# Optimization experiments

Measured on AMD Instinct MI355X. Metric: run time of the kernel, lower is better.

The kernel has to match this reference:

```python
import jax, jax.numpy as jnp
import numpy as np

B, S, DIN, DOUT = 4, 4096, 4096, 4096
W_SCALE = 0.02  # kaiming-ish scale; keeps values inside fp8 range


def setup_inputs() -> dict:
    key = jax.random.key(0)
    k1, k2, k3 = jax.random.split(key, 3)
    x = jax.random.normal(k1, (B, S, DIN), dtype=jnp.float16)
    weight = (jax.random.normal(k2, (DOUT, DIN), dtype=jnp.float32) * W_SCALE).astype(jnp.float16)
    bias = (jax.random.normal(k3, (DOUT,), dtype=jnp.float32) * W_SCALE).astype(jnp.float16)
    return {"x": x, "weight": weight, "bias": bias}


def reference(x, weight, bias):
    # Emulate torch._scaled_mm: activations quantized to fp8 e5m2,
    # weight (transposed) quantized to fp8 e4m3fn, scale_a = scale_b = 1.0,
    # accumulate in fp32, add fp16 bias, output fp16.
    out_shape = x.shape[:-1] + (weight.shape[0],)
    x8 = x.reshape(-1, x.shape[-1]).astype(jnp.float8_e5m2)       # [M, DIN]
    w8 = weight.T.astype(jnp.float8_e4m3fn)                        # [DIN, DOUT]
    scale = jnp.float32(1.0)  # scale_a * scale_b
    acc = jnp.matmul(x8.astype(jnp.float32), w8.astype(jnp.float32))  # [M, DOUT] fp32 accum
    out = (acc * scale + bias.astype(jnp.float32)).astype(jnp.float16)
    return out.reshape(out_shape)
```

## Files before the change

kernel.cpp:

```cpp
#include <hip/hip_runtime.h>
#include <hip/hip_fp16.h>

#define M_DIM 16384
#define N_DIM 4096
#define K_DIM 4096

typedef __attribute__((ext_vector_type(16))) float f32x16;
typedef __attribute__((ext_vector_type(4)))  int   i32x4;
typedef __attribute__((ext_vector_type(8)))  int   i32x8;

template<bool E4M3>
__global__ __launch_bounds__(256) void quant_tile_kernel(
    const float* __restrict__ in,
    uint4* __restrict__ out,
    int ngrp)
{
  int t = blockIdx.x * 256 + threadIdx.x;
  if (t >= ngrp) return;
  const int g    = t & 1023;
  const int tile = t >> 10;
  const int kt   = tile & 63;
  const int bt   = tile >> 6;
  const int sb   = g >> 7;
  const int half = (g >> 6) & 1;
  const int l    = g & 63;
  const int row  = bt * 256 + sb * 32 + (l & 31);
  const int k    = kt * 64 + (l >> 5) * 32 + half * 16;

  const float4* p = reinterpret_cast<const float4*>(in + (size_t)row * K_DIM + k);
  float4 v0 = p[0], v1 = p[1], v2 = p[2], v3 = p[3];
  int w0 = 0, w1 = 0, w2 = 0, w3 = 0;
  if (E4M3) {
    w0 = __builtin_amdgcn_cvt_pk_fp8_f32(v0.x, v0.y, w0, false);
    w0 = __builtin_amdgcn_cvt_pk_fp8_f32(v0.z, v0.w, w0, true);
    w1 = __builtin_amdgcn_cvt_pk_fp8_f32(v1.x, v1.y, w1, false);
    w1 = __builtin_amdgcn_cvt_pk_fp8_f32(v1.z, v1.w, w1, true);
    w2 = __builtin_amdgcn_cvt_pk_fp8_f32(v2.x, v2.y, w2, false);
    w2 = __builtin_amdgcn_cvt_pk_fp8_f32(v2.z, v2.w, w2, true);
    w3 = __builtin_amdgcn_cvt_pk_fp8_f32(v3.x, v3.y, w3, false);
    w3 = __builtin_amdgcn_cvt_pk_fp8_f32(v3.z, v3.w, w3, true);
  } else {
    w0 = __builtin_amdgcn_cvt_pk_bf8_f32(v0.x, v0.y, w0, false);
    w0 = __builtin_amdgcn_cvt_pk_bf8_f32(v0.z, v0.w, w0, true);
    w1 = __builtin_amdgcn_cvt_pk_bf8_f32(v1.x, v1.y, w1, false);
    w1 = __builtin_amdgcn_cvt_pk_bf8_f32(v1.z, v1.w, w1, true);
    w2 = __builtin_amdgcn_cvt_pk_bf8_f32(v2.x, v2.y, w2, false);
    w2 = __builtin_amdgcn_cvt_pk_bf8_f32(v2.z, v2.w, w2, true);
    w3 = __builtin_amdgcn_cvt_pk_bf8_f32(v3.x, v3.y, w3, false);
    w3 = __builtin_amdgcn_cvt_pk_bf8_f32(v3.z, v3.w, w3, true);
  }
  out[t] = make_uint4((unsigned)w0, (unsigned)w1, (unsigned)w2, (unsigned)w3);
}

__global__ __launch_bounds__(512, 2) void gemm_fp8_kernel(
    const unsigned char* __restrict__ Aq,
    const unsigned char* __restrict__ Wq,
    const float* __restrict__ bias,
    float* __restrict__ C)
{
  __shared__ __align__(16) unsigned char lds[98304];

  const int tid  = threadIdx.x;
  const int lane = tid & 63;
  const int wave = tid >> 6;
  const int wr   = wave >> 2;
  const int wc   = wave & 3;

  const int bid = blockIdx.x;
  const int swz = (bid & 7) * 128 + (bid >> 3);
  const int bmi = swz >> 4;
  const int bni = swz & 15;

  const unsigned char* tA = Aq + (size_t)bmi * (64 * 16384);
  const unsigned char* tB = Wq + (size_t)bni * (64 * 16384);

  const size_t t16 = (size_t)tid * 16;
  const int    w1k = wave * 1024;

#define STAGE(gb, lo_)                                                      \
  __builtin_amdgcn_global_load_lds(                                        \
      (const __attribute__((address_space(1))) void*)((gb) + t16),          \
      (__attribute__((address_space(3))) void*)(lds + (lo_) + w1k), 16, 0, 0)

#define RD8(dst, off)                                                       \
  { const unsigned char* _p = lds + (off) + lane * 16;                      \
    union { i32x8 v; i32x4 h[2]; } _u;                                      \
    _u.h[0] = *(const i32x4*)_p;                                            \
    _u.h[1] = *(const i32x4*)(_p + 1024);                                   \
    (dst) = _u.v; }

#define MFMA(d, a, b)                                                       \
  d = __builtin_amdgcn_mfma_scale_f32_32x32x64_f8f6f4(                      \
      a, b, d, 1 , 0 , 0, 0x7F7F7F7F, 0, 0x7F7F7F7F)

#define SBAR __builtin_amdgcn_sched_barrier(0)
#define BAR  __builtin_amdgcn_s_barrier()
#define DSW  asm volatile("s_waitcnt lgkmcnt(0)" ::: "memory"); SBAR
#define VMW4 asm volatile("s_waitcnt vmcnt(4)" ::: "memory"); SBAR
#define P1   __builtin_amdgcn_s_setprio(1)
#define P0   __builtin_amdgcn_s_setprio(0)

  const int aoff = wr * 8192;
  const int boff = 16384 + wc * 4096;

  f32x16 acc[4][2] = {};
  i32x8 aU, aV, bE0, bE1, bO0, bO1;

  STAGE(tA,         0);      STAGE(tA + 8192,  8192);
  STAGE(tB,         16384);  STAGE(tB + 8192,  24576);
  SBAR;
  STAGE(tA + 16384, 32768);  STAGE(tA + 24576, 40960);
  STAGE(tB + 16384, 49152);  STAGE(tB + 24576, 57344);
  SBAR;
  VMW4;
  BAR;

  int cA = 0, cB = 32768, cC = 65536;

  for (int it = 0; it < 32; ++it) {
    const int t = it << 1;
    const size_t tpC = (size_t)((t + 2) & 63) * 16384;
    const size_t tpD = (size_t)((t + 3) & 63) * 16384;

    RD8(bE0, cA + boff);  RD8(bE1, cA + boff + 2048);
    RD8(aU,  cA + aoff);
    STAGE(tA + tpC, cC);
    BAR; DSW; P1;
    MFMA(acc[0][0], aU, bE0); MFMA(acc[0][1], aU, bE1);
    P0; BAR;
    RD8(aV, cA + aoff + 2048);
    STAGE(tA + tpC + 8192, cC + 8192);
    BAR; DSW; P1;
    MFMA(acc[1][0], aV, bE0); MFMA(acc[1][1], aV, bE1);
    P0; BAR;
    RD8(aU, cA + aoff + 4096);
    STAGE(tB + tpC, cC + 16384);
    BAR; DSW; P1;
    MFMA(acc[2][0], aU, bE0); MFMA(acc[2][1], aU, bE1);
    P0; BAR;
    RD8(aV, cA + aoff + 6144);
    STAGE(tB + tpC + 8192, cC + 24576);
    BAR; DSW; P1;
    MFMA(acc[3][0], aV, bE0); MFMA(acc[3][1], aV, bE1);
    P0;
    VMW4;
    BAR;

    RD8(bO0, cB + boff);  RD8(bO1, cB + boff + 2048);
    RD8(aU,  cB + aoff);
    STAGE(tA + tpD, cA);
    BAR; DSW; P1;
    MFMA(acc[0][0], aU, bO0); MFMA(acc[0][1], aU, bO1);
    P0; BAR;
    RD8(aV, cB + aoff + 2048);
    STAGE(tA + tpD + 8192, cA + 8192);
    BAR; DSW; P1;
    MFMA(acc[1][0], aV, bO0); MFMA(acc[1][1], aV, bO1);
    P0; BAR;
    RD8(aU, cB + aoff + 4096);
    STAGE(tB + tpD, cA + 16384);
    BAR; DSW; P1;
    MFMA(acc[2][0], aU, bO0); MFMA(acc[2][1], aU, bO1);
    P0; BAR;
    RD8(aV, cB + aoff + 6144);
    STAGE(tB + tpD + 8192, cA + 24576);
    BAR; DSW; P1;
    MFMA(acc[3][0], aV, bO0); MFMA(acc[3][1], aV, bO1);
    P0;
    VMW4;
    BAR;

    const int nA = cC, nB = cA, nC = cB;
    cA = nA; cB = nB; cC = nC;
  }
#undef STAGE
#undef RD8
#undef MFMA
#undef SBAR
#undef BAR
#undef DSW
#undef VMW4
#undef P1
#undef P0

  #pragma unroll
  for (int n = 0; n < 2; ++n) {
    const int col = bni * 256 + wc * 64 + n * 32 + (lane & 31);
    const float bv = bias[col];
    #pragma unroll
    for (int m = 0; m < 4; ++m) {
      const int rbase = bmi * 256 + wr * 128 + m * 32 + ((lane >> 5) << 2);
      #pragma unroll
      for (int r = 0; r < 16; ++r) {
        const int row = rbase + (r & 3) + 8 * (r >> 2);
        C[(size_t)row * N_DIM + col] =
            __half2float(__float2half_rn(acc[m][n][r] + bv));
      }
    }
  }
}

extern "C" void kernel_launch(void* const* d_in, const int* in_sizes, int n_in,
                              void* d_out, int out_size, void* d_ws, size_t ws_size,
                              hipStream_t stream) {
  const float* x  = (const float*)d_in[0];
  const float* w  = (const float*)d_in[1];
  const float* bs = (const float*)d_in[2];
  float* out = (float*)d_out;

  unsigned char* xq = (unsigned char*)d_ws;
  unsigned char* wq = (unsigned char*)d_ws + (size_t)M_DIM * K_DIM;

  const int ngx = (M_DIM * K_DIM) / 16;
  const int ngw = (N_DIM * K_DIM) / 16;
  quant_tile_kernel<false><<<ngx / 256, 256, 0, stream>>>(x, (uint4*)xq, ngx);
  quant_tile_kernel<true ><<<ngw / 256, 256, 0, stream>>>(w, (uint4*)wq, ngw);

  gemm_fp8_kernel<<<1024, 512, 0, stream>>>(xq, wq, bs, out);
}
```

Measured before the change: 353.7 us.

## Load B fragments directly from global into registers and collapse per-phase barriers

```diff
diff --git a/kernel.cpp b/kernel.cpp
--- a/kernel.cpp
+++ b/kernel.cpp
@@ -8,6 +8,8 @@
 typedef __attribute__((ext_vector_type(16))) float f32x16;
 typedef __attribute__((ext_vector_type(4)))  int   i32x4;
 typedef __attribute__((ext_vector_type(8)))  int   i32x8;
+
+union frag_u { i32x8 v; i32x4 h[2]; };
 
 template<bool E4M3>
 __global__ __launch_bounds__(256) void quant_tile_kernel(
@@ -58,7 +60,7 @@
     const float* __restrict__ bias,
     float* __restrict__ C)
 {
-  __shared__ __align__(16) unsigned char lds[98304];
+  __shared__ __align__(16) unsigned char lds[49152];
 
   const int tid  = threadIdx.x;
   const int lane = tid & 63;
@@ -76,6 +78,7 @@
 
   const size_t t16 = (size_t)tid * 16;
   const int    w1k = wave * 1024;
+  const unsigned char* gbp = tB + wc * 4096 + lane * 16;
 
 #define STAGE(gb, lo_)                                                      \
   __builtin_amdgcn_global_load_lds(                                        \
@@ -84,102 +87,84 @@
 
 #define RD8(dst, off)                                                       \
   { const unsigned char* _p = lds + (off) + lane * 16;                      \
-    union { i32x8 v; i32x4 h[2]; } _u;                                      \
-    _u.h[0] = *(const i32x4*)_p;                                            \
-    _u.h[1] = *(const i32x4*)(_p + 1024);                                   \
-    (dst) = _u.v; }
+    (dst).h[0] = *reinterpret_cast<const i32x4*>(_p);                       \
+    (dst).h[1] = *reinterpret_cast<const i32x4*>(_p + 1024); }
+
+#define LDB(dst, p)                                                         \
+  { (dst).h[0] = *reinterpret_cast<const i32x4*>(p);                        \
+    (dst).h[1] = *reinterpret_cast<const i32x4*>((p) + 1024); }
 
 #define MFMA(d, a, b)                                                       \
   d = __builtin_amdgcn_mfma_scale_f32_32x32x64_f8f6f4(                      \
       a, b, d, 1 , 0 , 0, 0x7F7F7F7F, 0, 0x7F7F7F7F)
 
 #define SBAR __builtin_amdgcn_sched_barrier(0)
-#define BAR  __builtin_amdgcn_s_barrier()
-#define DSW  asm volatile("s_waitcnt lgkmcnt(0)" ::: "memory"); SBAR
-#define VMW4 asm volatile("s_waitcnt vmcnt(4)" ::: "memory"); SBAR
+#define BAR  { SBAR; __builtin_amdgcn_s_barrier(); SBAR; }
+#define VMW6 { asm volatile("s_waitcnt vmcnt(6)" ::: "memory"); SBAR; }
 #define P1   __builtin_amdgcn_s_setprio(1)
 #define P0   __builtin_amdgcn_s_setprio(0)
 
   const int aoff = wr * 8192;
-  const int boff = 16384 + wc * 4096;
 
   f32x16 acc[4][2] = {};
-  i32x8 aU, aV, bE0, bE1, bO0, bO1;
-
-  STAGE(tA,         0);      STAGE(tA + 8192,  8192);
-  STAGE(tB,         16384);  STAGE(tB + 8192,  24576);
+  frag_u a0, a1, a2, a3, bE0, bE1, bO0, bO1;
+
+  STAGE(tA, 0); STAGE(tA + 8192, 8192);
   SBAR;
-  STAGE(tA + 16384, 32768);  STAGE(tA + 24576, 40960);
-  STAGE(tB + 16384, 49152);  STAGE(tB + 24576, 57344);
+  LDB(bE0, gbp); LDB(bE1, gbp + 2048);
+  STAGE(tA + 16384, 16384); STAGE(tA + 24576, 24576);
   SBAR;
-  VMW4;
+  VMW6;
   BAR;
 
-  int cA = 0, cB = 32768, cC = 65536;
+  int cA = 0, cB = 16384, cC = 32768;
 
   for (int it = 0; it < 32; ++it) {
     const int t = it << 1;
-    const size_t tpC = (size_t)((t + 2) & 63) * 16384;
-    const size_t tpD = (size_t)((t + 3) & 63) * 16384;
-
-    RD8(bE0, cA + boff);  RD8(bE1, cA + boff + 2048);
-    RD8(aU,  cA + aoff);
-    STAGE(tA + tpC, cC);
-    BAR; DSW; P1;
-    MFMA(acc[0][0], aU, bE0); MFMA(acc[0][1], aU, bE1);
-    P0; BAR;
-    RD8(aV, cA + aoff + 2048);
-    STAGE(tA + tpC + 8192, cC + 8192);
-    BAR; DSW; P1;
-    MFMA(acc[1][0], aV, bE0); MFMA(acc[1][1], aV, bE1);
-    P0; BAR;
-    RD8(aU, cA + aoff + 4096);
-    STAGE(tB + tpC, cC + 16384);
-    BAR; DSW; P1;
-    MFMA(acc[2][0], aU, bE0); MFMA(acc[2][1], aU, bE1);
-    P0; BAR;
-    RD8(aV, cA + aoff + 6144);
-    STAGE(tB + tpC + 8192, cC + 24576);
-    BAR; DSW; P1;
-    MFMA(acc[3][0], aV, bE0); MFMA(acc[3][1], aV, bE1);
-    P0;
-    VMW4;
-    BAR;
-
-    RD8(bO0, cB + boff);  RD8(bO1, cB + boff + 2048);
-    RD8(aU,  cB + aoff);
-    STAGE(tA + tpD, cA);
-    BAR; DSW; P1;
-    MFMA(acc[0][0], aU, bO0); MFMA(acc[0][1], aU, bO1);
-    P0; BAR;
-    RD8(aV, cB + aoff + 2048);
-    STAGE(tA + tpD + 8192, cA + 8192);
-    BAR; DSW; P1;
-    MFMA(acc[1][0], aV, bO0); MFMA(acc[1][1], aV, bO1);
-    P0; BAR;
-    RD8(aU, cB + aoff + 4096);
-    STAGE(tB + tpD, cA + 16384);
-    BAR; DSW; P1;
-    MFMA(acc[2][0], aU, bO0); MFMA(acc[2][1], aU, bO1);
-    P0; BAR;
-    RD8(aV, cB + aoff + 6144);
-    STAGE(tB + tpD + 8192, cA + 24576);
-    BAR; DSW; P1;
-    MFMA(acc[3][0], aV, bO0); MFMA(acc[3][1], aV, bO1);
-    P0;
-    VMW4;
-    BAR;
-
+    {
+      const size_t tpB = (size_t)((t + 1) & 63) * 16384;
+      const size_t tpA = (size_t)((t + 2) & 63) * 16384;
+      LDB(bO0, gbp + tpB); LDB(bO1, gbp + tpB + 2048);
+      STAGE(tA + tpA, cC); STAGE(tA + tpA + 8192, cC + 8192);
+      SBAR;
+      RD8(a0, cA + aoff);        RD8(a1, cA + aoff + 2048);
+      RD8(a2, cA + aoff + 4096); RD8(a3, cA + aoff + 6144);
+      P1;
+      MFMA(acc[0][0], a0.v, bE0.v); MFMA(acc[0][1], a0.v, bE1.v);
+      MFMA(acc[1][0], a1.v, bE0.v); MFMA(acc[1][1], a1.v, bE1.v);
+      MFMA(acc[2][0], a2.v, bE0.v); MFMA(acc[2][1], a2.v, bE1.v);
+      MFMA(acc[3][0], a3.v, bE0.v); MFMA(acc[3][1], a3.v, bE1.v);
+      P0;
+      VMW6;
+      BAR;
+    }
+    {
+      const size_t tpB = (size_t)((t + 2) & 63) * 16384;
+      const size_t tpA = (size_t)((t + 3) & 63) * 16384;
+      LDB(bE0, gbp + tpB); LDB(bE1, gbp + tpB + 2048);
+      STAGE(tA + tpA, cA); STAGE(tA + tpA + 8192, cA + 8192);
+      SBAR;
+      RD8(a0, cB + aoff);        RD8(a1, cB + aoff + 2048);
+      RD8(a2, cB + aoff + 4096); RD8(a3, cB + aoff + 6144);
+      P1;
+      MFMA(acc[0][0], a0.v, bO0.v); MFMA(acc[0][1], a0.v, bO1.v);
+      MFMA(acc[1][0], a1.v, bO0.v); MFMA(acc[1][1], a1.v, bO1.v);
+      MFMA(acc[2][0], a2.v, bO0.v); MFMA(acc[2][1], a2.v, bO1.v);
+      MFMA(acc[3][0], a3.v, bO0.v); MFMA(acc[3][1], a3.v, bO1.v);
+      P0;
+      VMW6;
+      BAR;
+    }
     const int nA = cC, nB = cA, nC = cB;
     cA = nA; cB = nB; cC = nC;
   }
 #undef STAGE
 #undef RD8
+#undef LDB
 #undef MFMA
 #undef SBAR
 #undef BAR
-#undef DSW
-#undef VMW4
+#undef VMW6
 #undef P1
 #undef P0
 
```

New measurement: 411.8 us. 16.4% more time.
